# Optimization experiments

Measured on AMD Instinct MI355X. Metric: run time of the kernel, lower is better.

Reference implementation:

```python
import jax, jax.numpy as jnp
import numpy as np

N = 100000
E = 3200000
CH_IN = 128
HID = 128
CH_OUT = 3


def setup_inputs() -> dict:
    key = jax.random.key(0)
    ks = jax.random.split(key, 16)
    def lin(kw, fan_in, fan_out):
        bound = 1.0 / np.sqrt(fan_in)
        kw1, kw2 = jax.random.split(kw)
        W = jax.random.uniform(kw1, (fan_in, fan_out), jnp.float32, -bound, bound)
        b = jax.random.uniform(kw2, (fan_out,), jnp.float32, -bound, bound)
        return W, b
    x = jax.random.normal(ks[0], (N, CH_IN), jnp.float32)
    edge_index = jax.random.randint(ks[1], (2, E), 0, N, jnp.int64)
    W1, b1 = lin(ks[2], CH_IN, HID)
    W2, b2 = lin(ks[3], HID, HID)
    lw1, lb1 = lin(ks[4], HID, HID)
    lw2, lb2 = lin(ks[5], HID, HID)
    lw3, lb3 = lin(ks[6], HID, HID)
    lw4, lb4 = lin(ks[7], HID, CH_OUT)
    return {"x": x, "edge_index": edge_index,
            "W1": W1, "b1": b1, "W2": W2, "b2": b2,
            "lw1": lw1, "lb1": lb1, "lw2": lw2, "lb2": lb2,
            "lw3": lw3, "lb3": lb3, "lw4": lw4, "lb4": lb4}


def gcn_conv(x, W, b, src, dst, n_nodes):
    xw = x @ W  # [N, H]
    ew = jnp.ones(src.shape[0], x.dtype)
    deg = jax.ops.segment_sum(ew, dst, num_segments=n_nodes) + 2.0  # +2 from improved self-loop
    dinv = jnp.where(deg > 0, jax.lax.rsqrt(deg), 0.0)
    norm = dinv[src] * dinv[dst]  # [E]
    agg = jax.ops.segment_sum(xw[src] * norm[:, None], dst, num_segments=n_nodes)
    # self-loop contribution: weight 2 * dinv[i]^2 * xw[i]
    agg = agg + xw * (2.0 * dinv * dinv)[:, None]
    return agg + b


def reference(x, edge_index, W1, b1, W2, b2, lw1, lb1, lw2, lb2, lw3, lb3, lw4, lb4):
    src, dst = edge_index[0], edge_index[1]
    n = x.shape[0]
    h = jnp.tanh(gcn_conv(x, W1, b1, src, dst, n))
    h = jnp.tanh(gcn_conv(h, W2, b2, src, dst, n))
    # dropout in eval mode = identity
    h = jnp.tanh(h @ lw1 + lb1)
    h = jnp.tanh(h @ lw2 + lb2)
    h = jnp.tanh(h @ lw3 + lb3)
    return h @ lw4 + lb4
```

## Files before the change

kernel.cpp:

```cpp
#include <hip/hip_runtime.h>

typedef __attribute__((ext_vector_type(8))) short short8;
typedef __attribute__((ext_vector_type(4))) float floatx4;
typedef __attribute__((ext_vector_type(4))) unsigned int uintx4;
typedef unsigned int uint32;

__device__ inline float b2f(unsigned short u) {
    union { uint32 i; float f; } x; x.i = ((uint32)u) << 16; return x.f;
}
__device__ inline float bl(uint32 v) {
    union { uint32 i; float f; } x; x.i = v << 16; return x.f;
}
__device__ inline float bh(uint32 v) {
    union { uint32 i; float f; } x; x.i = v & 0xffff0000u; return x.f;
}
__device__ inline unsigned short f2b(float f) {
    union { float f; uint32 u; } x; x.f = f;
    uint32 r = x.u + 0x7fffu + ((x.u >> 16) & 1u);
    return (unsigned short)(r >> 16);
}
__device__ inline float fast_tanh(float x) {
    float ax = __builtin_fabsf(x);
    float t = __builtin_amdgcn_exp2f(-2.8853900817779268f * ax);
    float r = (1.0f - t) * __builtin_amdgcn_rcpf(1.0f + t);
    return __builtin_copysignf(r, x);
}


#define CHUNK 8192
#define MAXBK 512
#define CAP   8704

__global__ __launch_bounds__(512, 2) void scatterb_k(const int* __restrict__ eidx,
                                                     uint32* __restrict__ bkt_cur,
                                                     uint32* __restrict__ packed, int E) {
    __shared__ uint32 hist[MAXBK];
    __shared__ uint32 ssum[MAXBK];
    __shared__ uint32 hsc[MAXBK];
    __shared__ uint32 gbase[MAXBK];
    __shared__ uint32 lcur[MAXBK];
    __shared__ uint32 stage[CHUNK];
    __shared__ unsigned short stgb[CHUNK];
    int t = threadIdx.x;
    int cbase = blockIdx.x * CHUNK;
    int n = E - cbase; if (n > CHUNK) n = CHUNK;

    hist[t] = 0;
    __syncthreads();
    int dreg[CHUNK / 512];
    int nt = 0;
    for (int i = t; i < n; i += 512) {
        int d = eidx[E + cbase + i];
        dreg[nt++] = d;
        atomicAdd(&hist[d >> 8], 1u);
    }
    __syncthreads();
    uint32 v = hist[t];
    ssum[t] = v;
    __syncthreads();
    for (int off = 1; off < MAXBK; off <<= 1) {
        uint32 x = (t >= off) ? ssum[t - off] : 0;
        __syncthreads();
        ssum[t] += x;
        __syncthreads();
    }
    uint32 excl = ssum[t] - v;
    hsc[t] = excl;
    lcur[t] = excl;
    if (v) gbase[t] = atomicAdd(&bkt_cur[t], v);
    __syncthreads();
    nt = 0;
    for (int i = t; i < n; i += 512) {
        int s = eidx[cbase + i];
        int d = dreg[nt++];
        int b = d >> 8;
        uint32 pos = atomicAdd(&lcur[b], 1u);
        stage[pos] = ((uint32)s << 8) | (uint32)(d & 255);
        stgb[pos] = (unsigned short)b;
    }
    __syncthreads();
    for (int i = t; i < n; i += 512) {
        int b = stgb[i];
        packed[gbase[b] + (i - hsc[b])] = stage[i];
    }
}

__global__ __launch_bounds__(256) void buildb_k(const uint32* __restrict__ packed,
                                                const uint32* __restrict__ bkt_cur,
                                                int* __restrict__ rowp,
                                                int* __restrict__ rowe,
                                                float* __restrict__ dinv,
                                                int* __restrict__ csr, int N) {
    __shared__ uint32 cnt[256];
    __shared__ uint32 incl[256];
    __shared__ uint32 cur[256];
    int t = threadIdx.x;
    int b = blockIdx.x;
    uint32 base = (uint32)b * CAP;
    uint32 size = bkt_cur[b] - base;
    int node0 = b << 8;

    cnt[t] = 0;
    __syncthreads();
    for (uint32 i = t; i < size; i += 256)
        atomicAdd(&cnt[packed[base + i] & 255u], 1u);
    __syncthreads();
    uint32 v = cnt[t];
    incl[t] = v;
    __syncthreads();
    for (int off = 1; off < 256; off <<= 1) {
        uint32 x = (t >= off) ? incl[t - off] : 0;
        __syncthreads();
        incl[t] += x;
        __syncthreads();
    }
    uint32 loc = incl[t] - v;
    cur[t] = loc;
    int node = node0 + t;
    if (node < N) {
        dinv[node] = rsqrtf((float)v + 2.0f);
        rowp[node] = (int)(base + loc);
        rowe[node] = (int)(base + loc + v);
    }
    __syncthreads();
    for (uint32 i = t; i < size; i += 256) {
        uint32 p = packed[base + i];
        uint32 pos = atomicAdd(&cur[p & 255u], 1u);
        csr[base + pos] = (int)(p >> 8);
    }
}


__global__ __launch_bounds__(256) void prep_w5_k(const float* __restrict__ w0,
                                                 const float* __restrict__ w1,
                                                 const float* __restrict__ w2,
                                                 const float* __restrict__ w3,
                                                 const float* __restrict__ w4,
                                                 unsigned short* __restrict__ Wt_hi,
                                                 unsigned short* __restrict__ Wt_lo,
                                                 uint32* __restrict__ bkt_cur) {
    if (blockIdx.x < 2) {
        int idx = blockIdx.x * 256 + threadIdx.x;
        bkt_cur[idx] = (uint32)idx * CAP;
    }
    int t = blockIdx.x * 256 + threadIdx.x;
    int widx = t >> 11;
    int f8 = t & 2047;
    const float* W;
    switch (widx) {
        case 0: W = w0; break;
        case 1: W = w1; break;
        case 2: W = w2; break;
        case 3: W = w3; break;
        default: W = w4; break;
    }
    int ct = f8 >> 8, kc = (f8 >> 6) & 3, quad = (f8 >> 4) & 3, r = f8 & 15;
    int c = ct * 16 + r;
    int kbase = kc * 32 + quad * 8;
    short8 hi8, lo8;
#pragma unroll
    for (int j = 0; j < 8; ++j) {
        float w = W[(kbase + j) * 128 + c];
        unsigned short h = f2b(w);
        hi8[j] = (short)h;
        lo8[j] = (short)f2b(w - b2f(h));
    }
    *(short8*)(Wt_hi + widx * 16384 + f8 * 8) = hi8;
    *(short8*)(Wt_lo + widx * 16384 + f8 * 8) = lo8;
}


template <int ASRC>
__global__ __launch_bounds__(256, 4) void gemm_z_k(
    const void* __restrict__ Asrc,
    const unsigned short* __restrict__ Wt_hi,
    const unsigned short* __restrict__ Wt_lo,
    const float* __restrict__ dinv,
    unsigned short* __restrict__ out, int N) {
    int tid = threadIdx.x;
    int wave = tid >> 6, lane = tid & 63;
    int quad = lane >> 4, r = lane & 15;
    int m32 = blockIdx.x * 128 + wave * 32;

    short8 af[2][4];
#pragma unroll
    for (int s = 0; s < 2; ++s) {
        int rowA = m32 + s * 16 + r;
        if (rowA >= N) rowA = N - 1;
        if (ASRC == 0) {
            const float4* Af = (const float4*)Asrc;
#pragma unroll
            for (int kc = 0; kc < 4; ++kc) {
                float4 p0 = Af[((size_t)rowA * 128 + kc * 32 + quad * 8) >> 2];
                float4 p1 = Af[(((size_t)rowA * 128 + kc * 32 + quad * 8) >> 2) + 1];
                short8 a;
                a[0] = (short)f2b(p0.x); a[1] = (short)f2b(p0.y);
                a[2] = (short)f2b(p0.z); a[3] = (short)f2b(p0.w);
                a[4] = (short)f2b(p1.x); a[5] = (short)f2b(p1.y);
                a[6] = (short)f2b(p1.z); a[7] = (short)f2b(p1.w);
                af[s][kc] = a;
            }
        } else {
            const short* Ap = (const short*)Asrc;
#pragma unroll
            for (int kc = 0; kc < 4; ++kc)
                af[s][kc] = *(const short8*)(Ap + (size_t)rowA * 128 + kc * 32 + quad * 8);
        }
    }

    float dv[2][4];
#pragma unroll
    for (int s = 0; s < 2; ++s)
#pragma unroll
        for (int reg = 0; reg < 4; ++reg) {
            int i = m32 + s * 16 + quad * 4 + reg;
            dv[s][reg] = dinv[i < N ? i : N - 1];
        }

    const short8* WhF = (const short8*)Wt_hi + lane;
    const short8* WlF = (const short8*)Wt_lo + lane;

#pragma unroll
    for (int ct = 0; ct < 8; ++ct) {
        int n = ct * 16 + r;
        floatx4 a0 = {0.f, 0.f, 0.f, 0.f}, a1 = {0.f, 0.f, 0.f, 0.f};
#pragma unroll
        for (int kc = 0; kc < 4; ++kc) {
            short8 bh8 = WhF[(ct * 4 + kc) << 6];
            a0 = __builtin_amdgcn_mfma_f32_16x16x32_bf16(af[0][kc], bh8, a0, 0, 0, 0);
            a1 = __builtin_amdgcn_mfma_f32_16x16x32_bf16(af[1][kc], bh8, a1, 0, 0, 0);
            short8 bl8 = WlF[(ct * 4 + kc) << 6];
            a0 = __builtin_amdgcn_mfma_f32_16x16x32_bf16(af[0][kc], bl8, a0, 0, 0, 0);
            a1 = __builtin_amdgcn_mfma_f32_16x16x32_bf16(af[1][kc], bl8, a1, 0, 0, 0);
        }
#pragma unroll
        for (int reg = 0; reg < 4; ++reg) {
            int i0 = m32 + quad * 4 + reg;
            if (i0 < N) out[(size_t)i0 * 128 + n] = f2b(a0[reg] * dv[0][reg]);
            int i1 = m32 + 16 + quad * 4 + reg;
            if (i1 < N) out[(size_t)i1 * 128 + n] = f2b(a1[reg] * dv[1][reg]);
        }
    }
}


#define LSTR 136

__global__ __launch_bounds__(256, 2) void mlp_fused_k(
    const unsigned short* __restrict__ H,
    const unsigned short* __restrict__ WH,
    const unsigned short* __restrict__ WL,
    const float* __restrict__ lb1, const float* __restrict__ lb2,
    const float* __restrict__ lb3,
    const float* __restrict__ W4, const float* __restrict__ b4,
    float* __restrict__ out, int N) {
    __shared__ __align__(16) unsigned short wbuf[16384];
    __shared__ __align__(16) unsigned short tile[4][32 * LSTR];
    __shared__ float w4s[384];
    int tid = threadIdx.x;
    if (tid < 192) { w4s[tid] = W4[tid]; w4s[tid + 192] = W4[tid + 192]; }

    int wave = tid >> 6, lane = tid & 63;
    int quad = lane >> 4, r = lane & 15;
    unsigned short* T = tile[wave];
    int m32 = blockIdx.x * 128 + wave * 32;

    short8 af[2][4];
    const short* Hp = (const short*)H;
#pragma unroll
    for (int s = 0; s < 2; ++s) {
        int rowA = m32 + s * 16 + r;
        if (rowA >= N) rowA = N - 1;
#pragma unroll
        for (int kc = 0; kc < 4; ++kc)
            af[s][kc] = *(const short8*)(Hp + (size_t)rowA * 128 + kc * 32 + quad * 8);
    }

    const float* biases[3] = {lb1, lb2, lb3};
#pragma unroll
    for (int L = 0; L < 3; ++L) {
        const float* bias = biases[L];
        float bvv[8];
#pragma unroll
        for (int ct = 0; ct < 8; ++ct) bvv[ct] = bias[ct * 16 + r];
#pragma unroll
        for (int hf = 0; hf < 2; ++hf) {
            __syncthreads();
            {
                const uintx4* sh = (const uintx4*)(WH + L * 16384 + hf * 8192);
                const uintx4* sl = (const uintx4*)(WL + L * 16384 + hf * 8192);
                uintx4* dh = (uintx4*)wbuf;
                uintx4* dl = (uintx4*)(wbuf + 8192);
#pragma unroll
                for (int it = 0; it < 4; ++it) dh[tid + it * 256] = sh[tid + it * 256];
#pragma unroll
                for (int it = 0; it < 4; ++it) dl[tid + it * 256] = sl[tid + it * 256];
            }
            __syncthreads();
            const short8* whF = (const short8*)wbuf + lane;
            const short8* wlF = (const short8*)(wbuf + 8192) + lane;
#pragma unroll
            for (int c2 = 0; c2 < 4; ++c2) {
                int ct = hf * 4 + c2;
                int n = ct * 16 + r;
                floatx4 a0 = {0.f, 0.f, 0.f, 0.f}, a1 = {0.f, 0.f, 0.f, 0.f};
#pragma unroll
                for (int kc = 0; kc < 4; ++kc) {
                    short8 bh8 = whF[(c2 * 4 + kc) << 6];
                    a0 = __builtin_amdgcn_mfma_f32_16x16x32_bf16(af[0][kc], bh8, a0, 0, 0, 0);
                    a1 = __builtin_amdgcn_mfma_f32_16x16x32_bf16(af[1][kc], bh8, a1, 0, 0, 0);
                    short8 bl8 = wlF[(c2 * 4 + kc) << 6];
                    a0 = __builtin_amdgcn_mfma_f32_16x16x32_bf16(af[0][kc], bl8, a0, 0, 0, 0);
                    a1 = __builtin_amdgcn_mfma_f32_16x16x32_bf16(af[1][kc], bl8, a1, 0, 0, 0);
                }
                float bv = bvv[ct];
#pragma unroll
                for (int reg = 0; reg < 4; ++reg) {
                    int lrow = quad * 4 + reg;
                    T[lrow * LSTR + n] = f2b(fast_tanh(a0[reg] + bv));
                    T[(lrow + 16) * LSTR + n] = f2b(fast_tanh(a1[reg] + bv));
                }
            }
        }
        if (L < 2) {
#pragma unroll
            for (int s = 0; s < 2; ++s)
#pragma unroll
                for (int kc = 0; kc < 4; ++kc)
                    af[s][kc] = *(const short8*)&T[(s * 16 + r) * LSTR + kc * 32 + quad * 8];
        }
    }

    int lrow = lane & 31;
    int halfc = lane >> 5;
    float a0 = 0.f, a1 = 0.f, a2 = 0.f;
#pragma unroll
    for (int c8 = 0; c8 < 8; ++c8) {
        int cbase = halfc * 64 + c8 * 8;
        short8 hv = *(const short8*)&T[lrow * LSTR + cbase];
#pragma unroll
        for (int j = 0; j < 8; ++j) {
            float xv = b2f((unsigned short)hv[j]);
            int ch = cbase + j;
            a0 = fmaf(xv, w4s[ch * 3 + 0], a0);
            a1 = fmaf(xv, w4s[ch * 3 + 1], a1);
            a2 = fmaf(xv, w4s[ch * 3 + 2], a2);
        }
    }
    a0 += __shfl_xor(a0, 32);
    a1 += __shfl_xor(a1, 32);
    a2 += __shfl_xor(a2, 32);
    if (halfc == 0) {
        int i = m32 + lrow;
        if (i < N) {
            out[(size_t)i * 3 + 0] = a0 + b4[0];
            out[(size_t)i * 3 + 1] = a1 + b4[1];
            out[(size_t)i * 3 + 2] = a2 + b4[2];
        }
    }
}


__global__ __launch_bounds__(256) void agg_full_k(
    const uint32* __restrict__ z, const int* __restrict__ rowp,
    const int* __restrict__ rowe, const int* __restrict__ csr,
    const float* __restrict__ dinv, const float* __restrict__ bias,
    uint32* __restrict__ out, int N) {
    int lane = threadIdx.x & 63;
    int i = blockIdx.x * 4 + (threadIdx.x >> 6);
    if (i >= N) return;
    int start = rowp[i], end = rowe[i];
    const uint32* zl = z + lane;
    float a0 = 0.f, a1 = 0.f;
    for (int e = start; e < end; e += 64) {
        int cnt = end - e;
        if (cnt > 64) cnt = 64;
        int s = (lane < cnt) ? csr[e + lane] : N;
        int mp = (cnt + 15) & ~15;
        for (int m = 0; m < mp; m += 16) {
            uint32 v[16];
#pragma unroll
            for (int p = 0; p < 16; ++p) {
                int sj = __shfl(s, m + p);
                v[p] = zl[(size_t)sj << 6];
            }
#pragma unroll
            for (int p = 0; p < 16; ++p) {
                a0 += bl(v[p]);
                a1 += bh(v[p]);
            }
        }
    }
    uint32 vi = zl[(size_t)i << 6];
    a0 += 2.f * bl(vi);
    a1 += 2.f * bh(vi);
    float di = dinv[i];
    float2 bv = ((const float2*)bias)[lane];
    float h0 = fast_tanh(fmaf(di, a0, bv.x));
    float h1 = fast_tanh(fmaf(di, a1, bv.y));
    out[((size_t)i << 6) + lane] = (uint32)f2b(h0) | ((uint32)f2b(h1) << 16);
}

extern "C" void kernel_launch(void* const* d_in, const int* in_sizes, int n_in,
                              void* d_out, int out_size, void* d_ws, size_t ws_size,
                              hipStream_t stream) {
    const float* x   = (const float*)d_in[0];
    const int* eidx  = (const int*)d_in[1];
    const float* W1  = (const float*)d_in[2];
    const float* b1  = (const float*)d_in[3];
    const float* W2  = (const float*)d_in[4];
    const float* b2  = (const float*)d_in[5];
    const float* lw1 = (const float*)d_in[6];
    const float* lb1 = (const float*)d_in[7];
    const float* lw2 = (const float*)d_in[8];
    const float* lb2 = (const float*)d_in[9];
    const float* lw3 = (const float*)d_in[10];
    const float* lb3 = (const float*)d_in[11];
    const float* lw4 = (const float*)d_in[12];
    const float* lb4 = (const float*)d_in[13];
    float* out = (float*)d_out;

    const int N = in_sizes[0] / 128;
    const int E = in_sizes[1] / 2;

    char* p = (char*)d_ws;
    auto alloc = [&](size_t bytes) -> void* {
        void* q = (void*)p;
        p += (bytes + 255) & ~(size_t)255;
        return q;
    };
    const int NBK = (N + 255) >> 8;
    float* dinv      = (float*)alloc((size_t)N * 4);
    int* rowp        = (int*)alloc((size_t)N * 4);
    int* rowe        = (int*)alloc((size_t)N * 4);
    uint32* bkt_cur  = (uint32*)alloc(MAXBK * 4);
    int* csr         = (int*)alloc((size_t)NBK * CAP * 4);
    unsigned short* Wt_hi = (unsigned short*)alloc(5 * 16384 * 2);
    unsigned short* Wt_lo = (unsigned short*)alloc(5 * 16384 * 2);
    unsigned short* bufA  = (unsigned short*)alloc((size_t)(N + 1) * 128 * 2);
    unsigned short* bufB  = (unsigned short*)alloc((size_t)(N + 1) * 128 * 2);
    uint32* packed = (uint32*)bufA;

    const int MB4 = (N + 127) / 128;
    const int AB  = (N + 3) / 4;
    const int NCH = (E + CHUNK - 1) / CHUNK;

    hipMemsetAsync(bufA + (size_t)N * 128, 0, 256, stream);
    prep_w5_k<<<40, 256, 0, stream>>>(W1, W2, lw1, lw2, lw3, Wt_hi, Wt_lo, bkt_cur);
    scatterb_k<<<NCH, 512, 0, stream>>>(eidx, bkt_cur, packed, E);
    buildb_k<<<NBK, 256, 0, stream>>>(packed, bkt_cur, rowp, rowe, dinv, csr, N);

    const unsigned short* WH = Wt_hi;
    const unsigned short* WL = Wt_lo;

    gemm_z_k<0><<<MB4, 256, 0, stream>>>(x, WH + 0 * 16384, WL + 0 * 16384, dinv, bufA, N);
    agg_full_k<<<AB, 256, 0, stream>>>((const uint32*)bufA, rowp, rowe, csr, dinv, b1,
                                       (uint32*)bufB, N);
    gemm_z_k<1><<<MB4, 256, 0, stream>>>(bufB, WH + 1 * 16384, WL + 1 * 16384, dinv, bufA, N);
    agg_full_k<<<AB, 256, 0, stream>>>((const uint32*)bufA, rowp, rowe, csr, dinv, b2,
                                       (uint32*)bufB, N);
    mlp_fused_k<<<MB4, 256, 0, stream>>>(bufB, WH + 2 * 16384, WL + 2 * 16384,
                                         lb1, lb2, lb3, lw4, lb4, out, N);
}
```

Baseline: 455.3 us.

## Column-block feature layout with XCD-affine persistent aggregation for first GCN layer

The first GEMM now writes its bf16 output in eight 16-column blocks (block-major, N+1 rows each), and a new persistent aggregation kernel processes one column block at a time. Each workgroup starts on the block matching its XCD id and pulls node chunks from a per-block atomic counter. The aim is for each XCD's L2 to hold a 3.2MB slice of features instead of the full table, which should reduce random-gather misses. The second GEMM reads this blocked layout. The padding-row memset is folded into the GEMM kernel, which also resets the counters. In exchange, each gather is only 32 bytes per row, and the work queue adds atomic and barrier overhead.

```diff
diff --git a/kernel.cpp b/kernel.cpp
--- a/kernel.cpp
+++ b/kernel.cpp
@@ -170,14 +170,25 @@
 }
 
 
-template <int ASRC>
+template <int ASRC, int OUTB>
 __global__ __launch_bounds__(256, 4) void gemm_z_k(
     const void* __restrict__ Asrc,
     const unsigned short* __restrict__ Wt_hi,
     const unsigned short* __restrict__ Wt_lo,
     const float* __restrict__ dinv,
+    uint32* __restrict__ ctr,
     unsigned short* __restrict__ out, int N) {
     int tid = threadIdx.x;
+    const size_t Np1 = (size_t)N + 1;
+    if (blockIdx.x == 0) {
+        uint32* o32 = (uint32*)out;
+        if (OUTB) {
+            if (tid < 64) o32[((size_t)(tid >> 3) * Np1 + N) * 8 + (tid & 7)] = 0;
+            if (tid >= 64 && tid < 72) ctr[tid - 64] = 0;
+        } else {
+            if (tid < 64) o32[(size_t)N * 64 + tid] = 0;
+        }
+    }
     int wave = tid >> 6, lane = tid & 63;
     int quad = lane >> 4, r = lane & 15;
     int m32 = blockIdx.x * 128 + wave * 32;
@@ -200,11 +211,18 @@
                 a[6] = (short)f2b(p1.z); a[7] = (short)f2b(p1.w);
                 af[s][kc] = a;
             }
+        } else if (ASRC == 1) {
+            const short* Ap = (const short*)Asrc;
+#pragma unroll
+            for (int kc = 0; kc < 4; ++kc)
+                af[s][kc] = *(const short8*)(Ap + (size_t)rowA * 128 + kc * 32 + quad * 8);
         } else {
             const short* Ap = (const short*)Asrc;
 #pragma unroll
-            for (int kc = 0; kc < 4; ++kc)
-                af[s][kc] = *(const short8*)(Ap + (size_t)rowA * 128 + kc * 32 + quad * 8);
+            for (int kc = 0; kc < 4; ++kc) {
+                int g = kc * 2 + (quad >> 1);
+                af[s][kc] = *(const short8*)(Ap + ((size_t)g * Np1 + rowA) * 16 + (quad & 1) * 8);
+            }
         }
     }
 
@@ -236,9 +254,15 @@
 #pragma unroll
         for (int reg = 0; reg < 4; ++reg) {
             int i0 = m32 + quad * 4 + reg;
-            if (i0 < N) out[(size_t)i0 * 128 + n] = f2b(a0[reg] * dv[0][reg]);
             int i1 = m32 + 16 + quad * 4 + reg;
-            if (i1 < N) out[(size_t)i1 * 128 + n] = f2b(a1[reg] * dv[1][reg]);
+            if (OUTB) {
+                int g = n >> 4, c = n & 15;
+                if (i0 < N) out[((size_t)g * Np1 + i0) * 16 + c] = f2b(a0[reg] * dv[0][reg]);
+                if (i1 < N) out[((size_t)g * Np1 + i1) * 16 + c] = f2b(a1[reg] * dv[1][reg]);
+            } else {
+                if (i0 < N) out[(size_t)i0 * 128 + n] = f2b(a0[reg] * dv[0][reg]);
+                if (i1 < N) out[(size_t)i1 * 128 + n] = f2b(a1[reg] * dv[1][reg]);
+            }
         }
     }
 }
@@ -401,6 +425,75 @@
     out[((size_t)i << 6) + lane] = (uint32)f2b(h0) | ((uint32)f2b(h1) << 16);
 }
 
+
+__global__ __launch_bounds__(256) void agg_blk_k(
+    const uint32* __restrict__ z, const int* __restrict__ rowp,
+    const int* __restrict__ rowe, const int* __restrict__ csr,
+    const float* __restrict__ dinv, const float* __restrict__ bias,
+    uint32* __restrict__ ctr, uint32* __restrict__ out, int N) {
+    __shared__ int sh_chunk;
+    int tid = threadIdx.x;
+    int wave = tid >> 6, lane = tid & 63;
+    int sg = lane >> 3, j = lane & 7;
+    uint32 xcd;
+    asm volatile("s_getreg_b32 %0, hwreg(20, 0, 32)" : "=s"(xcd));
+    int g = (int)(xcd & 7u);
+    const size_t Np1 = (size_t)N + 1;
+    const int chunks = (N + 7) >> 3;
+
+    for (int gi = 0; gi < 8; ++gi) {
+        int gg = (g + gi) & 7;
+        const uint32* zg = z + (size_t)gg * Np1 * 8;
+        float2 bv = ((const float2*)bias)[gg * 8 + j];
+        for (;;) {
+            if (tid == 0) sh_chunk = (int)atomicAdd(&ctr[gg], 1u);
+            __syncthreads();
+            int chunk = sh_chunk;
+            __syncthreads();
+            if (chunk >= chunks) break;
+#pragma unroll
+            for (int t = 0; t < 2; ++t) {
+                int i = (chunk << 3) + wave * 2 + t;
+                if (i >= N) continue;
+                int start = rowp[i], end = rowe[i];
+                float a0 = 0.f, a1 = 0.f;
+                for (int e = start; e < end; e += 64) {
+                    int cnt = end - e;
+                    if (cnt > 64) cnt = 64;
+                    int s = (lane < cnt) ? csr[e + lane] : N;
+                    int mp = (cnt + 31) & ~31;
+                    for (int m = 0; m < mp; m += 32) {
+                        int s0 = __shfl(s, m + sg);
+                        int s1 = __shfl(s, m + 8 + sg);
+                        int s2 = __shfl(s, m + 16 + sg);
+                        int s3 = __shfl(s, m + 24 + sg);
+                        uint32 v0 = zg[(size_t)s0 * 8 + j];
+                        uint32 v1 = zg[(size_t)s1 * 8 + j];
+                        uint32 v2 = zg[(size_t)s2 * 8 + j];
+                        uint32 v3 = zg[(size_t)s3 * 8 + j];
+                        a0 += bl(v0); a1 += bh(v0);
+                        a0 += bl(v1); a1 += bh(v1);
+                        a0 += bl(v2); a1 += bh(v2);
+                        a0 += bl(v3); a1 += bh(v3);
+                    }
+                }
+                a0 += __shfl_xor(a0, 8);  a1 += __shfl_xor(a1, 8);
+                a0 += __shfl_xor(a0, 16); a1 += __shfl_xor(a1, 16);
+                a0 += __shfl_xor(a0, 32); a1 += __shfl_xor(a1, 32);
+                uint32 vi = zg[(size_t)i * 8 + j];
+                a0 += 2.f * bl(vi);
+                a1 += 2.f * bh(vi);
+                float di = dinv[i];
+                float h0 = fast_tanh(fmaf(di, a0, bv.x));
+                float h1 = fast_tanh(fmaf(di, a1, bv.y));
+                if (sg == 0)
+                    out[((size_t)gg * Np1 + i) * 8 + j] =
+                        (uint32)f2b(h0) | ((uint32)f2b(h1) << 16);
+            }
+        }
+    }
+}
+
 extern "C" void kernel_launch(void* const* d_in, const int* in_sizes, int n_in,
                               void* d_out, int out_size, void* d_ws, size_t ws_size,
                               hipStream_t stream) {
@@ -434,6 +527,7 @@
     int* rowp        = (int*)alloc((size_t)N * 4);
     int* rowe        = (int*)alloc((size_t)N * 4);
     uint32* bkt_cur  = (uint32*)alloc(MAXBK * 4);
+    uint32* ctr      = (uint32*)alloc(64);
     int* csr         = (int*)alloc((size_t)NBK * CAP * 4);
     unsigned short* Wt_hi = (unsigned short*)alloc(5 * 16384 * 2);
     unsigned short* Wt_lo = (unsigned short*)alloc(5 * 16384 * 2);
@@ -445,7 +539,6 @@
     const int AB  = (N + 3) / 4;
     const int NCH = (E + CHUNK - 1) / CHUNK;
 
-    hipMemsetAsync(bufA + (size_t)N * 128, 0, 256, stream);
     prep_w5_k<<<40, 256, 0, stream>>>(W1, W2, lw1, lw2, lw3, Wt_hi, Wt_lo, bkt_cur);
     scatterb_k<<<NCH, 512, 0, stream>>>(eidx, bkt_cur, packed, E);
     buildb_k<<<NBK, 256, 0, stream>>>(packed, bkt_cur, rowp, rowe, dinv, csr, N);
@@ -453,10 +546,12 @@
     const unsigned short* WH = Wt_hi;
     const unsigned short* WL = Wt_lo;
 
-    gemm_z_k<0><<<MB4, 256, 0, stream>>>(x, WH + 0 * 16384, WL + 0 * 16384, dinv, bufA, N);
-    agg_full_k<<<AB, 256, 0, stream>>>((const uint32*)bufA, rowp, rowe, csr, dinv, b1,
-                                       (uint32*)bufB, N);
-    gemm_z_k<1><<<MB4, 256, 0, stream>>>(bufB, WH + 1 * 16384, WL + 1 * 16384, dinv, bufA, N);
+    gemm_z_k<0, 1><<<MB4, 256, 0, stream>>>(x, WH + 0 * 16384, WL + 0 * 16384, dinv, ctr,
+                                            bufA, N);
+    agg_blk_k<<<2048, 256, 0, stream>>>((const uint32*)bufA, rowp, rowe, csr, dinv, b1,
+                                        ctr, (uint32*)bufB, N);
+    gemm_z_k<2, 0><<<MB4, 256, 0, stream>>>(bufB, WH + 1 * 16384, WL + 1 * 16384, dinv, ctr,
+                                            bufA, N);
     agg_full_k<<<AB, 256, 0, stream>>>((const uint32*)bufA, rowp, rowe, csr, dinv, b2,
                                        (uint32*)bufB, N);
     mlp_fused_k<<<MB4, 256, 0, stream>>>(bufB, WH + 2 * 16384, WL + 2 * 16384,
```

Measured after the change: 1.689 ms. 271% more time.
